# Kernel tuning notes

Hardware: AMD Instinct MI355X
Metric: run time of the kernel (lower is better)

Reference implementation:

```python
import jax, jax.numpy as jnp
import numpy as np

D_MODEL = 512
H = 8
D_FF = 2048
EPS = 1e-6
NEG_INF = -1.0e9


def setup_inputs() -> dict:
    key = jax.random.key(0)
    ks = jax.random.split(key, 12)
    B, S, D, F = 8, 2048, D_MODEL, D_FF
    s = 0.02
    inp = {
        "x": jax.random.normal(ks[0], (B, S, D), jnp.float32),
        "src_mask": jnp.ones((B, 1, 1, S), jnp.int32),
        "w_q": jax.random.normal(ks[1], (D, D), jnp.float32) * s,
        "b_q": jnp.zeros((D,), jnp.float32),
        "w_k": jax.random.normal(ks[2], (D, D), jnp.float32) * s,
        "b_k": jnp.zeros((D,), jnp.float32),
        "w_v": jax.random.normal(ks[3], (D, D), jnp.float32) * s,
        "b_v": jnp.zeros((D,), jnp.float32),
        "w_o": jax.random.normal(ks[4], (D, D), jnp.float32) * s,
        "b_o": jnp.zeros((D,), jnp.float32),
        "w_1": jax.random.normal(ks[5], (F, D), jnp.float32) * s,
        "b_1": jnp.zeros((F,), jnp.float32),
        "w_2": jax.random.normal(ks[6], (D, F), jnp.float32) * s,
        "b_2": jnp.zeros((D,), jnp.float32),
    }
    return inp


def _layer_norm(x):
    # Matches torch: (x - mu) / sqrt(std**2 + eps), std is UNBIASED (ddof=1);
    # alpha/bias params exist in the module but are never applied in forward.
    mu = jnp.mean(x, axis=-1, keepdims=True)
    var = jnp.var(x, axis=-1, keepdims=True, ddof=1)
    return (x - mu) / jnp.sqrt(var + EPS)


def _mha(x, src_mask, w_q, b_q, w_k, b_k, w_v, b_v, w_o, b_o):
    B, S, D = x.shape
    d_k = D // H
    q = x @ w_q.T + b_q
    k = x @ w_k.T + b_k
    v = x @ w_v.T + b_v
    # (B, S, H, d_k) -> (B, H, S, d_k)
    q = q.reshape(B, S, H, d_k).transpose(0, 2, 1, 3)
    k = k.reshape(B, S, H, d_k).transpose(0, 2, 1, 3)
    v = v.reshape(B, S, H, d_k).transpose(0, 2, 1, 3)
    scores = jnp.einsum("bhqd,bhkd->bhqk", q, k) / jnp.sqrt(jnp.float32(d_k))
    scores = jnp.where(src_mask == 0, NEG_INF, scores)
    attn = jax.nn.softmax(scores, axis=-1)  # (B, H, S, S) materialized, as in source
    out = jnp.einsum("bhqk,bhkd->bhqd", attn, v)
    out = out.transpose(0, 2, 1, 3).reshape(B, S, D)
    return out @ w_o.T + b_o


def _ffn(x, w_1, b_1, w_2, b_2):
    return jax.nn.relu(x @ w_1.T + b_1) @ w_2.T + b_2


def reference(x, src_mask, w_q, b_q, w_k, b_k, w_v, b_v, w_o, b_o, w_1, b_1, w_2, b_2):
    # dropout prob = 0.0 -> identity (eval-equivalent)
    x1 = x + _mha(_layer_norm(x), src_mask, w_q, b_q, w_k, b_k, w_v, b_v, w_o, b_o)
    return x1 + _ffn(_layer_norm(x1), w_1, b_1, w_2, b_2)
```

## Files before the change

### kernel.cpp

```cpp
#include <hip/hip_runtime.h>
#include <hip/hip_bf16.h>

typedef unsigned short u16;
typedef __bf16 bf16x8 __attribute__((ext_vector_type(8)));
typedef __bf16 bf16x4 __attribute__((ext_vector_type(4)));
typedef unsigned int u32x4 __attribute__((ext_vector_type(4)));
typedef float f32x4 __attribute__((ext_vector_type(4)));

#define SEQ 2048
#define DMODEL 512
#define NHEAD 8
#define DFF 2048
#define NBATCH 8
#define MROWS (NBATCH * SEQ)

__device__ __forceinline__ u16 f2b(float f) {
    __hip_bfloat16 h = __float2bfloat16(f);
    u16 u;
    __builtin_memcpy(&u, &h, 2);
    return u;
}

__device__ __forceinline__ unsigned int pack2(float a, float b) {
    float2 f{a, b};
    __hip_bfloat162 h = __float22bfloat162_rn(f);
    unsigned int u;
    __builtin_memcpy(&u, &h, 4);
    return u;
}

__device__ __forceinline__ float ex2(float x) {
#if __has_builtin(__builtin_amdgcn_exp2f)
    return __builtin_amdgcn_exp2f(x);
#else
    return exp2f(x);
#endif
}

__device__ __forceinline__ void gload_lds16(const void* g, void* lds) {
    auto* gp = reinterpret_cast<const __attribute__((address_space(1))) unsigned int*>(
        reinterpret_cast<uintptr_t>(g));
    auto* lp = reinterpret_cast<__attribute__((address_space(3))) unsigned int*>(
        reinterpret_cast<uintptr_t>(lds));
    __builtin_amdgcn_global_load_lds(gp, lp, 16, 0, 0);
}

__global__ __launch_bounds__(256) void cast_weights(
    const float* __restrict__ w0, const float* __restrict__ w1,
    const float* __restrict__ w2, const float* __restrict__ w3,
    const float* __restrict__ w4, const float* __restrict__ w5,
    u16* __restrict__ d0, u16* __restrict__ d1, u16* __restrict__ d2,
    u16* __restrict__ d3, u16* __restrict__ d4, u16* __restrict__ d5) {
    int blk = blockIdx.x;
    const float* s;
    u16* d;
    int base;
    if (blk < 512) {
        int seg = blk >> 7, lb = blk & 127;
        s = seg == 0 ? w0 : seg == 1 ? w1 : seg == 2 ? w2 : w3;
        d = seg == 0 ? d0 : seg == 1 ? d1 : seg == 2 ? d2 : d3;
        base = lb * 2048;
    } else if (blk < 1024) {
        s = w4; d = d4; base = (blk - 512) * 2048;
    } else {
        s = w5; d = d5; base = (blk - 1024) * 2048;
    }
    int i = base + threadIdx.x * 8;
    float4 a = *reinterpret_cast<const float4*>(s + i);
    float4 b = *reinterpret_cast<const float4*>(s + i + 4);
    ushort4 oa, ob;
    oa.x = f2b(a.x); oa.y = f2b(a.y); oa.z = f2b(a.z); oa.w = f2b(a.w);
    ob.x = f2b(b.x); ob.y = f2b(b.y); ob.z = f2b(b.z); ob.w = f2b(b.w);
    *reinterpret_cast<ushort4*>(d + i) = oa;
    *reinterpret_cast<ushort4*>(d + i + 4) = ob;
}

__global__ __launch_bounds__(256) void concat_bias(const float* __restrict__ bq,
                                                   const float* __restrict__ bk,
                                                   const float* __restrict__ bv,
                                                   float* __restrict__ dst) {
    int i = blockIdx.x * 256 + threadIdx.x;
    float v = i < 512 ? bq[i] : (i < 1024 ? bk[i - 512] : bv[i - 1024]);
    dst[i] = v;
}

__global__ __launch_bounds__(256) void ln_rows(const float* __restrict__ x,
                                               u16* __restrict__ out) {
    int row = blockIdx.x * 4 + (threadIdx.x >> 6);
    int l = threadIdx.x & 63;
    const float* xr = x + (size_t)row * DMODEL + l * 8;
    float4 a = *reinterpret_cast<const float4*>(xr);
    float4 b = *reinterpret_cast<const float4*>(xr + 4);
    float s = a.x + a.y + a.z + a.w + b.x + b.y + b.z + b.w;
    float q = a.x * a.x + a.y * a.y + a.z * a.z + a.w * a.w +
              b.x * b.x + b.y * b.y + b.z * b.z + b.w * b.w;
#pragma unroll
    for (int d = 32; d >= 1; d >>= 1) {
        s += __shfl_xor(s, d, 64);
        q += __shfl_xor(q, d, 64);
    }
    float mean = s * (1.f / 512.f);
    float var = (q - 512.f * mean * mean) * (1.f / 511.f);
    float rs = rsqrtf(var + 1e-6f);
    ushort4 o0, o1;
    o0.x = f2b((a.x - mean) * rs); o0.y = f2b((a.y - mean) * rs);
    o0.z = f2b((a.z - mean) * rs); o0.w = f2b((a.w - mean) * rs);
    o1.x = f2b((b.x - mean) * rs); o1.y = f2b((b.y - mean) * rs);
    o1.z = f2b((b.z - mean) * rs); o1.w = f2b((b.w - mean) * rs);
    u16* op = out + (size_t)row * DMODEL + l * 8;
    *reinterpret_cast<ushort4*>(op) = o0;
    *reinterpret_cast<ushort4*>(op + 4) = o1;
}

template <bool RELU, bool RESID, int OUTMODE>
__global__ __launch_bounds__(256, 2) void gemm_nt(
    const u16* __restrict__ A, const u16* __restrict__ W,
    const float* __restrict__ bias, const float* __restrict__ resid,
    void* __restrict__ Cout, void* __restrict__ Cout2, int N, int K) {
    __shared__ u16 Als[128 * 64];
    __shared__ u16 Bls[128 * 64];
    const int tid = threadIdx.x;
    const int l = tid & 63, w = tid >> 6;
    const int m0 = blockIdx.y * 128;
    const int n0 = blockIdx.x * 128;
    const int wr = (w >> 1) * 64, wc = (w & 1) * 64;
    const int lhi = l >> 4, l15 = l & 15, l7 = l & 7;

    f32x4 acc[4][4] = {};

    const int srow = l >> 3;
    const int scol = ((l & 7) * 8) ^ (srow << 3);

    for (int kt = 0; kt < K; kt += 64) {
        __syncthreads();
#pragma unroll
        for (int i = 0; i < 4; ++i) {
            int cc = w * 4 + i;
            int grow = cc * 8 + srow;
            gload_lds16(&A[(size_t)(m0 + grow) * K + kt + scol], &Als[cc * 512]);
            gload_lds16(&W[(size_t)(n0 + grow) * K + kt + scol], &Bls[cc * 512]);
        }
        __syncthreads();
#pragma unroll
        for (int kk = 0; kk < 2; ++kk) {
            const int koff = (kk * 32 + lhi * 8) ^ (l7 << 3);
            bf16x8 af[4], bfr[4];
#pragma unroll
            for (int m = 0; m < 4; ++m)
                af[m] = *reinterpret_cast<const bf16x8*>(
                    &Als[(wr + m * 16 + l15) * 64 + koff]);
#pragma unroll
            for (int n = 0; n < 4; ++n)
                bfr[n] = *reinterpret_cast<const bf16x8*>(
                    &Bls[(wc + n * 16 + l15) * 64 + koff]);
#pragma unroll
            for (int m = 0; m < 4; ++m)
#pragma unroll
                for (int n = 0; n < 4; ++n)
                    acc[m][n] = __builtin_amdgcn_mfma_f32_16x16x32_bf16(
                        af[m], bfr[n], acc[m][n], 0, 0, 0);
        }
    }

    int colg[4];
    float bv[4];
#pragma unroll
    for (int cn = 0; cn < 4; ++cn) {
        colg[cn] = n0 + wc + cn * 16 + l15;
        bv[cn] = bias[colg[cn]];
    }
#pragma unroll
    for (int am = 0; am < 4; ++am) {
        int rowg = m0 + wr + am * 16 + 4 * lhi;
#pragma unroll
        for (int cn = 0; cn < 4; ++cn) {
            float v[4];
#pragma unroll
            for (int r = 0; r < 4; ++r) {
                float t = acc[am][cn][r] + bv[cn];
                if constexpr (RELU) t = fmaxf(t, 0.f);
                if constexpr (RESID)
                    t += resid[(size_t)(rowg + r) * N + colg[cn]];
                v[r] = t;
            }
            if constexpr (OUTMODE == 0) {
                u16* o = (u16*)Cout;
#pragma unroll
                for (int r = 0; r < 4; ++r)
                    o[(size_t)(rowg + r) * N + colg[cn]] = f2b(v[r]);
            } else if constexpr (OUTMODE == 1) {
                float* o = (float*)Cout;
#pragma unroll
                for (int r = 0; r < 4; ++r)
                    o[(size_t)(rowg + r) * N + colg[cn]] = v[r];
            } else {
                if (n0 < 1024) {
                    u16* o = (u16*)Cout;
#pragma unroll
                    for (int r = 0; r < 4; ++r)
                        o[(size_t)(rowg + r) * 1024 + colg[cn]] = f2b(v[r]);
                } else {
                    u16* o = (u16*)Cout2;
                    int bb = rowg >> 11, sloc = rowg & 2047;
                    int dg = colg[cn] - 1024;
                    ushort4 pk;
                    pk.x = f2b(v[0]); pk.y = f2b(v[1]);
                    pk.z = f2b(v[2]); pk.w = f2b(v[3]);
                    *reinterpret_cast<ushort4*>(
                        &o[(size_t)bb * 1048576 + (size_t)(sloc >> 2) * 2048 +
                           dg * 4]) = pk;
                }
            }
        }
    }
}

__global__ __launch_bounds__(256, 3) void attn_fwd(
    const u16* __restrict__ qk, const u16* __restrict__ v4,
    const int* __restrict__ mask, u16* __restrict__ out) {
    __shared__ u16 Kls[2][64 * 64];
    __shared__ u16 Vls[2][64 * 64];
    const int tid = threadIdx.x;
    const int l = tid & 63, w = tid >> 6;
    const int lhi = l >> 4, l15 = l & 15;
    const int lb = (blockIdx.x & 7) * 128 + (blockIdx.x >> 3);
    const int qt = lb & 15, bh = lb >> 4;
    const int b = bh >> 3, h = bh & 7;
    const int q0 = qt * 128 + w * 32;

    const u16* Qb = qk + (size_t)b * SEQ * 1024 + h * 64;
    const u16* Kb = Qb + 512;
    const u16* Vb4 = v4 + (size_t)b * 1048576 + h * 256;
    const int* Mb = mask + b * SEQ;

    const int srow = l >> 3;
    const int scol = ((l & 7) ^ srow) << 3;

    bf16x8 qf[2][2];
#pragma unroll
    for (int g = 0; g < 2; ++g) {
        size_t qa = (size_t)(q0 + g * 16 + l15) * 1024 + lhi * 8;
        qf[g][0] = *reinterpret_cast<const bf16x8*>(&Qb[qa]);
        qf[g][1] = *reinterpret_cast<const bf16x8*>(&Qb[qa + 32]);
    }

    int allone;
    {
        int acc = 1;
#pragma unroll
        for (int i = 0; i < 8; ++i) {
            int4 mm = *reinterpret_cast<const int4*>(&Mb[l * 32 + i * 4]);
            acc &= mm.x & mm.y & mm.z & mm.w;
        }
        allone = __all(acc == 1);
    }

    float lrun[2] = {0.f, 0.f};
    f32x4 oacc[2][4] = {};
    const float C1 = 0.18033688f;

    auto stage = [&](int buf, int kv) {
#pragma unroll
        for (int i = 0; i < 2; ++i) {
            int cc = w * 2 + i;
            int row = cc * 8 + srow;
            gload_lds16(&Kb[(size_t)(kv + row) * 1024 + scol], &Kls[buf][cc * 512]);
            gload_lds16(&Vb4[(size_t)((kv >> 2) + cc * 2 + (l >> 5)) * 2048 +
                             (l & 31) * 8],
                        &Vls[buf][cc * 512]);
        }
    };

    stage(0, 0);
    asm volatile("s_waitcnt vmcnt(0)" ::: "memory");
    __builtin_amdgcn_s_barrier();

    for (int t = 0; t < 32; ++t) {
        const int buf = t & 1;
        const int kv = t * 64;
        if (t < 31) stage(buf ^ 1, kv + 64);
        __builtin_amdgcn_sched_barrier(0);

        const int sw = (l15 & 7) << 3;

        f32x4 sc[2][4];
        __builtin_amdgcn_s_setprio(1);
#pragma unroll
        for (int ks = 0; ks < 4; ++ks) {
            int krow = ks * 16 + l15;
            bf16x8 ka0 = *reinterpret_cast<const bf16x8*>(
                &Kls[buf][krow * 64 + ((lhi * 8) ^ sw)]);
            bf16x8 ka1 = *reinterpret_cast<const bf16x8*>(
                &Kls[buf][krow * 64 + ((32 + lhi * 8) ^ sw)]);
#pragma unroll
            for (int g = 0; g < 2; ++g) {
                f32x4 z = {};
                z = __builtin_amdgcn_mfma_f32_16x16x32_bf16(ka0, qf[g][0], z, 0, 0, 0);
                z = __builtin_amdgcn_mfma_f32_16x16x32_bf16(ka1, qf[g][1], z, 0, 0, 0);
                sc[g][ks] = z;
            }
        }
        __builtin_amdgcn_s_setprio(0);

        if (!allone) {
            int4 mm[4];
#pragma unroll
            for (int ks = 0; ks < 4; ++ks)
                mm[ks] = *reinterpret_cast<const int4*>(&Mb[kv + ks * 16 + 4 * lhi]);
#pragma unroll
            for (int ks = 0; ks < 4; ++ks) {
                if (mm[ks].x == 0) { sc[0][ks][0] = -3e38f; sc[1][ks][0] = -3e38f; }
                if (mm[ks].y == 0) { sc[0][ks][1] = -3e38f; sc[1][ks][1] = -3e38f; }
                if (mm[ks].z == 0) { sc[0][ks][2] = -3e38f; sc[1][ks][2] = -3e38f; }
                if (mm[ks].w == 0) { sc[0][ks][3] = -3e38f; sc[1][ks][3] = -3e38f; }
            }
        }

        u32x4 pku[2][2];
#pragma unroll
        for (int g = 0; g < 2; ++g) {
            float ps = 0.f;
#pragma unroll
            for (int ks = 0; ks < 4; ++ks) {
                float p0 = ex2(fminf(sc[g][ks][0] * C1, 30.f));
                float p1 = ex2(fminf(sc[g][ks][1] * C1, 30.f));
                float p2 = ex2(fminf(sc[g][ks][2] * C1, 30.f));
                float p3 = ex2(fminf(sc[g][ks][3] * C1, 30.f));
                ps += (p0 + p1) + (p2 + p3);
                pku[g][ks >> 1][(ks & 1) * 2 + 0] = pack2(p0, p1);
                pku[g][ks >> 1][(ks & 1) * 2 + 1] = pack2(p2, p3);
            }
            ps += __shfl_xor(ps, 16, 64);
            ps += __shfl_xor(ps, 32, 64);
            lrun[g] += ps;
        }

        __builtin_amdgcn_s_setprio(1);
#pragma unroll
        for (int kp = 0; kp < 2; ++kp) {
#pragma unroll
            for (int dc = 0; dc < 4; ++dc) {
                int dl4 = (dc * 16 + l15) * 4;
                bf16x4 v0 = *reinterpret_cast<const bf16x4*>(
                    &Vls[buf][(kp * 8 + lhi) * 256 + dl4]);
                bf16x4 v1 = *reinterpret_cast<const bf16x4*>(
                    &Vls[buf][(kp * 8 + 4 + lhi) * 256 + dl4]);
                bf16x8 vb8;
                vb8[0] = v0[0]; vb8[1] = v0[1]; vb8[2] = v0[2]; vb8[3] = v0[3];
                vb8[4] = v1[0]; vb8[5] = v1[1]; vb8[6] = v1[2]; vb8[7] = v1[3];
#pragma unroll
                for (int g = 0; g < 2; ++g)
                    oacc[g][dc] = __builtin_amdgcn_mfma_f32_16x16x32_bf16(
                        __builtin_bit_cast(bf16x8, pku[g][kp]), vb8, oacc[g][dc],
                        0, 0, 0);
            }
        }
        __builtin_amdgcn_s_setprio(0);

        asm volatile("s_waitcnt vmcnt(0)" ::: "memory");
        __builtin_amdgcn_s_barrier();
    }

#pragma unroll
    for (int g = 0; g < 2; ++g) {
        float inv = 1.f / lrun[g];
        float invr[4];
#pragma unroll
        for (int r = 0; r < 4; ++r) invr[r] = __shfl(inv, 4 * lhi + r, 16);
#pragma unroll
        for (int r = 0; r < 4; ++r) {
            size_t rowa =
                ((size_t)b * SEQ + q0 + g * 16 + 4 * lhi + r) * DMODEL + h * 64;
#pragma unroll
            for (int dc = 0; dc < 4; ++dc)
                out[rowa + dc * 16 + l15] = f2b(oacc[g][dc][r] * invr[r]);
        }
    }
}

extern "C" void kernel_launch(void* const* d_in, const int* in_sizes, int n_in,
                              void* d_out, int out_size, void* d_ws,
                              size_t ws_size, hipStream_t stream) {
    const float* x = (const float*)d_in[0];
    const int* mask = (const int*)d_in[1];
    const float* w_q = (const float*)d_in[2];
    const float* b_q = (const float*)d_in[3];
    const float* w_k = (const float*)d_in[4];
    const float* b_k = (const float*)d_in[5];
    const float* w_v = (const float*)d_in[6];
    const float* b_v = (const float*)d_in[7];
    const float* w_o = (const float*)d_in[8];
    const float* b_o = (const float*)d_in[9];
    const float* w_1 = (const float*)d_in[10];
    const float* b_1 = (const float*)d_in[11];
    const float* w_2 = (const float*)d_in[12];
    const float* b_2 = (const float*)d_in[13];

    char* ws = (char*)d_ws;
    const size_t MB = 1024ull * 1024ull;
    u16* lnx = (u16*)(ws + 0);
    u16* qkb = (u16*)(ws + 16 * MB);
    u16* v4 = (u16*)(ws + 48 * MB);
    u16* lnx1 = (u16*)(ws + 16 * MB);
    u16* hbuf = (u16*)(ws + 32 * MB);
    u16* wqkv = (u16*)(ws + 96 * MB);
    u16* wob = wqkv + 3 * 262144;
    u16* w1b = wqkv + 4 * 262144;
    u16* w2b = w1b + 1048576;
    float* bqkv = (float*)(w2b + 1048576);
    u16* attn_o = lnx;
    float* x1 = (float*)d_out;

    cast_weights<<<1536, 256, 0, stream>>>(
        w_q, w_k, w_v, w_o, w_1, w_2, wqkv, wqkv + 262144, wqkv + 2 * 262144,
        wob, w1b, w2b);
    concat_bias<<<6, 256, 0, stream>>>(b_q, b_k, b_v, bqkv);
    ln_rows<<<4096, 256, 0, stream>>>(x, lnx);

    dim3 g12(12, 128), g4(4, 128), g16(16, 128);
    gemm_nt<false, false, 3><<<g12, 256, 0, stream>>>(lnx, wqkv, bqkv, nullptr,
                                                      qkb, v4, 1536, 512);
    attn_fwd<<<1024, 256, 0, stream>>>(qkb, v4, mask, attn_o);
    gemm_nt<false, true, 1><<<g4, 256, 0, stream>>>(attn_o, wob, b_o, x, x1,
                                                    nullptr, 512, 512);
    ln_rows<<<4096, 256, 0, stream>>>(x1, lnx1);
    gemm_nt<true, false, 0><<<g16, 256, 0, stream>>>(lnx1, w1b, b_1, nullptr,
                                                     hbuf, nullptr, 2048, 512);
    gemm_nt<false, true, 1><<<g4, 256, 0, stream>>>(hbuf, w2b, b_2, x1,
                                                    (float*)d_out, nullptr,
                                                    512, 2048);
}
```

Baseline: 283.3 us.

## Fold softmax scale into Q weights, unroll attention loop by two, raise occupancy

Pre-multiplies the Q projection weights and bias by the log2e/sqrt(d_k) constant during the bf16 cast, so the attention inner loop no longer multiplies each score before exp2. The KV loop is manually unrolled by two so buffer indices become compile-time constants. Launch bounds for attn_fwd are raised from 3 to 4 waves per SIMD, which may force register spills. Q is now stored scaled in bf16, which changes rounding slightly.

```diff
diff --git a/kernel.cpp b/kernel.cpp
--- a/kernel.cpp
+++ b/kernel.cpp
@@ -13,6 +13,8 @@
 #define DFF 2048
 #define NBATCH 8
 #define MROWS (NBATCH * SEQ)
+
+#define C1_FOLD 0.18033688f
 
 __device__ __forceinline__ u16 f2b(float f) {
     __hip_bfloat16 h = __float2bfloat16(f);
@@ -55,11 +57,13 @@
     const float* s;
     u16* d;
     int base;
+    float sc = 1.0f;
     if (blk < 512) {
         int seg = blk >> 7, lb = blk & 127;
         s = seg == 0 ? w0 : seg == 1 ? w1 : seg == 2 ? w2 : w3;
         d = seg == 0 ? d0 : seg == 1 ? d1 : seg == 2 ? d2 : d3;
         base = lb * 2048;
+        if (seg == 0) sc = C1_FOLD;
     } else if (blk < 1024) {
         s = w4; d = d4; base = (blk - 512) * 2048;
     } else {
@@ -69,8 +73,10 @@
     float4 a = *reinterpret_cast<const float4*>(s + i);
     float4 b = *reinterpret_cast<const float4*>(s + i + 4);
     ushort4 oa, ob;
-    oa.x = f2b(a.x); oa.y = f2b(a.y); oa.z = f2b(a.z); oa.w = f2b(a.w);
-    ob.x = f2b(b.x); ob.y = f2b(b.y); ob.z = f2b(b.z); ob.w = f2b(b.w);
+    oa.x = f2b(a.x * sc); oa.y = f2b(a.y * sc);
+    oa.z = f2b(a.z * sc); oa.w = f2b(a.w * sc);
+    ob.x = f2b(b.x * sc); ob.y = f2b(b.y * sc);
+    ob.z = f2b(b.z * sc); ob.w = f2b(b.w * sc);
     *reinterpret_cast<ushort4*>(d + i) = oa;
     *reinterpret_cast<ushort4*>(d + i + 4) = ob;
 }
@@ -80,7 +86,7 @@
                                                    const float* __restrict__ bv,
                                                    float* __restrict__ dst) {
     int i = blockIdx.x * 256 + threadIdx.x;
-    float v = i < 512 ? bq[i] : (i < 1024 ? bk[i - 512] : bv[i - 1024]);
+    float v = i < 512 ? bq[i] * C1_FOLD : (i < 1024 ? bk[i - 512] : bv[i - 1024]);
     dst[i] = v;
 }
 
@@ -215,7 +221,7 @@
     }
 }
 
-__global__ __launch_bounds__(256, 3) void attn_fwd(
+__global__ __launch_bounds__(256, 4) void attn_fwd(
     const u16* __restrict__ qk, const u16* __restrict__ v4,
     const int* __restrict__ mask, u16* __restrict__ out) {
     __shared__ u16 Kls[2][64 * 64];
@@ -257,7 +263,6 @@
 
     float lrun[2] = {0.f, 0.f};
     f32x4 oacc[2][4] = {};
-    const float C1 = 0.18033688f;
 
     auto stage = [&](int buf, int kv) {
 #pragma unroll
@@ -271,17 +276,11 @@
         }
     };
 
-    stage(0, 0);
-    asm volatile("s_waitcnt vmcnt(0)" ::: "memory");
-    __builtin_amdgcn_s_barrier();
-
-    for (int t = 0; t < 32; ++t) {
-        const int buf = t & 1;
-        const int kv = t * 64;
-        if (t < 31) stage(buf ^ 1, kv + 64);
+    const int sw = (l15 & 7) << 3;
+
+    auto tile = [&](int buf, int kv, bool pf, int pbuf, int pkv) {
+        if (pf) stage(pbuf, pkv);
         __builtin_amdgcn_sched_barrier(0);
-
-        const int sw = (l15 & 7) << 3;
 
         f32x4 sc[2][4];
         __builtin_amdgcn_s_setprio(1);
@@ -322,10 +321,10 @@
             float ps = 0.f;
 #pragma unroll
             for (int ks = 0; ks < 4; ++ks) {
-                float p0 = ex2(fminf(sc[g][ks][0] * C1, 30.f));
-                float p1 = ex2(fminf(sc[g][ks][1] * C1, 30.f));
-                float p2 = ex2(fminf(sc[g][ks][2] * C1, 30.f));
-                float p3 = ex2(fminf(sc[g][ks][3] * C1, 30.f));
+                float p0 = ex2(fminf(sc[g][ks][0], 30.f));
+                float p1 = ex2(fminf(sc[g][ks][1], 30.f));
+                float p2 = ex2(fminf(sc[g][ks][2], 30.f));
+                float p3 = ex2(fminf(sc[g][ks][3], 30.f));
                 ps += (p0 + p1) + (p2 + p3);
                 pku[g][ks >> 1][(ks & 1) * 2 + 0] = pack2(p0, p1);
                 pku[g][ks >> 1][(ks & 1) * 2 + 1] = pack2(p2, p3);
@@ -359,6 +358,16 @@
 
         asm volatile("s_waitcnt vmcnt(0)" ::: "memory");
         __builtin_amdgcn_s_barrier();
+    };
+
+    stage(0, 0);
+    asm volatile("s_waitcnt vmcnt(0)" ::: "memory");
+    __builtin_amdgcn_s_barrier();
+
+    for (int tt = 0; tt < 16; ++tt) {
+        const int base = tt * 128;
+        tile(0, base, true, 1, base + 64);
+        tile(1, base + 64, tt < 15, 0, base + 128);
     }
 
 #pragma unroll
```

Result: slower. 290.0 us (+2.4%).
